# Performance work log

Measured on AMD Instinct MI355X. Metric: run time of the kernel, lower is better.

Reference implementation:

```python
import jax, jax.numpy as jnp
import numpy as np
from jax import lax

FIRE_RATE = 0.5       # forward() default fire_rate
INPUT_CHANNELS = 1    # module input_channels
EPS = 1e-5            # BatchNorm eps


def p4_conv_z2(x, w, b):
    """Z2 -> P4 group conv. x: [B,I,H,W], w: [O,I,k,k] -> [B,O,4,H,W]."""
    # rotate the spatial kernel by r*90deg for each of the 4 output orientations
    ws = jnp.stack([jnp.rot90(w, r, axes=(2, 3)) for r in range(4)], axis=1)  # [O,4,I,k,k]
    O, _, I, k, _ = ws.shape
    y = lax.conv_general_dilated(x, ws.reshape(O * 4, I, k, k), (1, 1), 'SAME',
                                 dimension_numbers=('NCHW', 'OIHW', 'NCHW'))
    B, _, H, W = x.shape
    return y.reshape(B, O, 4, H, W) + b[None, :, None, None, None]


def p4_conv_p4(x, w, b):
    """P4 -> P4 group conv. x: [B,I,4,H,W], w: [O,I,4,k,k] -> [B,O,4,H,W]."""
    # for output orientation r: cyclic-shift input-orientation axis by r and rotate spatially by r
    ws = jnp.stack([jnp.rot90(jnp.roll(w, r, axis=2), r, axes=(3, 4)) for r in range(4)],
                   axis=1)  # [O,4,I,4,k,k]
    O, _, I, _, k, _ = ws.shape
    B, _, _, H, W = x.shape
    y = lax.conv_general_dilated(x.reshape(B, I * 4, H, W),
                                 ws.reshape(O * 4, I * 4, k, k), (1, 1), 'SAME',
                                 dimension_numbers=('NCHW', 'OIHW', 'NCHW'))
    return y.reshape(B, O, 4, H, W) + b[None, :, None, None, None]


def _update(x_nhwc, w1, b1, gamma, beta, w2, b2, key):
    x = jnp.transpose(x_nhwc, (0, 3, 1, 2))            # [B,C,H,W]
    y = p4_conv_z2(x, w1, b1)                          # [B,Ch,4,H,W]
    # BatchNorm3d (batch stats, affine): normalize each channel over (B, rot, H, W)
    mu = jnp.mean(y, axis=(0, 2, 3, 4), keepdims=True)
    var = jnp.var(y, axis=(0, 2, 3, 4), keepdims=True)
    y = gamma[None, :, None, None, None] * (y - mu) * lax.rsqrt(var + EPS) \
        + beta[None, :, None, None, None]
    y = jax.nn.relu(y)
    dy = p4_conv_p4(y, w2, b2).mean(axis=2)            # mean over rotation axis -> [B,C,H,W]
    B, _, H, W = dy.shape
    mask = (jax.random.uniform(key, (B, 1, H, W), dtype=dy.dtype) > FIRE_RATE).astype(dy.dtype)
    x = x + dy * mask
    return jnp.transpose(x, (0, 2, 3, 1))              # back to [B,H,W,C]


def nca_forward(x, w1, b1, gamma, beta, w2, b2, steps):
    base_key = jax.random.key(42)
    for step in range(steps):
        x2 = _update(x, w1, b1, gamma, beta, w2, b2, jax.random.fold_in(base_key, step))
        # first input_channels are clamped to the original input
        x = jnp.concatenate((x[..., :INPUT_CHANNELS], x2[..., INPUT_CHANNELS:]), axis=-1)
    return x


def setup_inputs() -> dict:
    key = jax.random.key(0)
    ks = jax.random.split(key, 6)
    B, H, W = 8, 192, 192
    C = 16            # channel_n
    CH = 128 // 8     # base_hidden_size = hidden_size // 8
    K = 7             # kernel_size
    # fan-in scaled init (matches nn.Conv2d-style scaling)
    x = jax.random.normal(ks[0], (B, H, W, C), dtype=jnp.float32)
    w1 = jax.random.normal(ks[1], (CH, C, K, K), dtype=jnp.float32) / np.sqrt(C * K * K)
    b1 = jnp.zeros((CH,), dtype=jnp.float32)
    gamma = jnp.ones((CH,), dtype=jnp.float32)
    beta = jnp.zeros((CH,), dtype=jnp.float32)
    w2 = jax.random.normal(ks[2], (C, CH, 4, 1, 1), dtype=jnp.float32) / np.sqrt(CH * 4)
    b2 = jnp.zeros((C,), dtype=jnp.float32)
    return {"x": x, "w1": w1, "b1": b1, "gamma": gamma, "beta": beta,
            "w2": w2, "b2": b2, "steps": 10}


def reference(x, w1, b1, gamma, beta, w2, b2, steps):
    return nca_forward(x, w1, b1, gamma, beta, w2, b2, steps)
```

## Files before the change

kernel.cpp:

```cpp
#include <hip/hip_runtime.h>
#include <stdint.h>

#define HH 192
#define WW 192
#define BB 8
#define NSTEP 10
#define HWSZ (HH*WW)
#define NPIX (BB*HWSZ)
#define TILE_W 24
#define TILE_H 16
#define XROWS 22
#define XCOLS 30
#define RSU   488
#define XBUFU (XROWS*RSU)
#define NKS   25
#define NBLK  (8*12*8)

typedef _Float16 f16x8 __attribute__((ext_vector_type(8)));
typedef float    f32x4 __attribute__((ext_vector_type(4)));

typedef __attribute__((address_space(1))) const uint32_t glb_u32;
typedef __attribute__((address_space(3))) uint32_t lds_u32;

union PackU { ushort u[8]; uint4 v; };

__host__ __device__ inline void tf2x32(uint32_t k0, uint32_t k1,
                                       uint32_t x0, uint32_t x1,
                                       uint32_t &o0, uint32_t &o1) {
  const uint32_t k2 = k0 ^ k1 ^ 0x1BD11BDAu;
  x0 += k0; x1 += k1;
#define TFR(r) { x0 += x1; x1 = (x1 << (r)) | (x1 >> (32 - (r))); x1 ^= x0; }
  TFR(13) TFR(15) TFR(26) TFR(6)
  x0 += k1; x1 += k2 + 1u;
  TFR(17) TFR(29) TFR(16) TFR(24)
  x0 += k2; x1 += k0 + 2u;
  TFR(13) TFR(15) TFR(26) TFR(6)
  x0 += k0; x1 += k1 + 3u;
  TFR(17) TFR(29) TFR(16) TFR(24)
  x0 += k1; x1 += k2 + 4u;
  TFR(13) TFR(15) TFR(26) TFR(6)
  x0 += k2; x1 += k0 + 5u;
#undef TFR
  o0 = x0; o1 = x1;
}

__device__ inline void split2048(float v, ushort &h, ushort &l) {
  _Float16 hi = (_Float16)v;
  float r = (v - (float)hi) * 2048.0f;
  _Float16 lo = (_Float16)r;
  h = __builtin_bit_cast(ushort, hi);
  l = __builtin_bit_cast(ushort, lo);
}

__global__ void k_prep_wfrag(const float* __restrict__ w1,
                             ushort* __restrict__ wfh, ushort* __restrict__ wfl) {
  int idx = blockIdx.x * 256 + threadIdx.x;
  if (idx >= NKS * 4 * 64) return;
  const int lane = idx & 63;
  const int sm = idx >> 6;
  const int s = sm >> 2, mt = sm & 3;
  const int m = lane & 15, g = lane >> 4;
  const int j = mt * 16 + m, co = j >> 2, r = j & 3;
  const int t = 2 * s + (g >> 1);
  PackU ph, pl;
#pragma unroll
  for (int e = 0; e < 8; ++e) {
    const int ci = 8 * (g & 1) + e;
    float wv = 0.f;
    if (t < 49) {
      const int ky = t / 7, kx = t - (t / 7) * 7;
      int a = ky, b = kx;
      for (int i = 0; i < r; ++i) { int na = b, nb = 6 - a; a = na; b = nb; }
      wv = w1[((co * 16 + ci) * 7 + a) * 7 + b];
    }
    split2048(wv, ph.u[e], pl.u[e]);
  }
  ((uint4*)wfh)[sm * 64 + lane] = ph.v;
  ((uint4*)wfl)[sm * 64 + lane] = pl.v;
}

__global__ void k_prep_w2(const float* __restrict__ w2, float* __restrict__ wsum) {
  int idx = threadIdx.x;
  float s = 0.f;
  for (int t = 0; t < 4; ++t) s += w2[idx * 4 + t];
  wsum[idx] = 0.25f * s;
}

__global__ __launch_bounds__(512, 2) void k_conv1(
    const float* __restrict__ xsrc,
    const ushort* __restrict__ wfh,
    const ushort* __restrict__ wfl,
    const float* __restrict__ b1,
    float* __restrict__ y,
    float* __restrict__ partials)
{
  __shared__ __align__(16) ushort xsm[2 * XBUFU];
  __shared__ __align__(16) ushort abh[2][2048];
  __shared__ __align__(16) ushort abl[2][2048];
  __shared__ float red2[8][32];
  const int tid = threadIdx.x;
  const int lane = tid & 63, wid = tid >> 6;
  const int x0 = blockIdx.x * TILE_W, y0 = blockIdx.y * TILE_H;
  const int b = blockIdx.z;

  {
    const ushort* gsrc = ((wid < 4) ? wfh : wfl) + (wid & 3) * 512 + lane * 8;
    ushort* ldst = ((wid < 4) ? abh[0] : abl[0]) + (wid & 3) * 512;
    __builtin_amdgcn_global_load_lds((glb_u32*)gsrc, (lds_u32*)ldst, 16, 0, 0);
  }

  for (int p = tid; p < XROWS * XCOLS * 2; p += 512) {
    const int half = p & 1, t2 = p >> 1;
    const int lr = t2 / XCOLS, lc = t2 - (t2 / XCOLS) * XCOLS;
    const int gy = y0 + lr - 3, gx = x0 + lc - 3;
    float4 v0, v1;
    if ((unsigned)gy < (unsigned)HH && (unsigned)gx < (unsigned)WW) {
      const float4* px = (const float4*)(xsrc + ((size_t)b * HWSZ + (size_t)gy * WW + gx) * 16 + half * 8);
      v0 = px[0]; v1 = px[1];
    } else {
      v0 = v1 = make_float4(0.f, 0.f, 0.f, 0.f);
    }
    const float xv[8] = {v0.x, v0.y, v0.z, v0.w, v1.x, v1.y, v1.z, v1.w};
    PackU h, l;
#pragma unroll
    for (int c = 0; c < 8; ++c) split2048(xv[c], h.u[c], l.u[c]);
    const int ub = lr * RSU + lc * 16 + half * 8;
    *(uint4*)&xsm[ub] = h.v;
    *(uint4*)&xsm[XBUFU + ub] = l.v;
  }
  __syncthreads();

  const int n = lane & 15;
  const int q = lane >> 4;
  const int h = q & 1;
  const int bU0 = n * RSU + (3 * wid + 0) * 16 + h * 8;
  const int bU1 = bU0 + 16;
  const int bU2 = bU0 + 32;

  float bias[4];
#pragma unroll
  for (int mt = 0; mt < 4; ++mt) bias[mt] = b1[mt * 4 + q];

  f32x4 accH[3][4], accC[3][4];
#pragma unroll
  for (int st = 0; st < 3; ++st)
#pragma unroll
    for (int mt = 0; mt < 4; ++mt) {
      const float bv = bias[mt];
      accH[st][mt] = (f32x4){bv, bv, bv, bv};
      accC[st][mt] = (f32x4){0.f, 0.f, 0.f, 0.f};
    }

  f16x8 Ah[4], Al[4];
  f16x8 Bh[2][3], Bl[2][3];

  {
    const int off = (lane < 32) ? 0 : 16;
    Bh[0][0] = *(const f16x8*)&xsm[bU0 + off];
    Bl[0][0] = *(const f16x8*)&xsm[XBUFU + bU0 + off];
    Bh[0][1] = *(const f16x8*)&xsm[bU1 + off];
    Bl[0][1] = *(const f16x8*)&xsm[XBUFU + bU1 + off];
    Bh[0][2] = *(const f16x8*)&xsm[bU2 + off];
    Bl[0][2] = *(const f16x8*)&xsm[XBUFU + bU2 + off];
  }

#pragma unroll
  for (int s = 0; s < NKS; ++s) {
    const int cb = s & 1, nb = cb ^ 1;
    if (s < NKS - 1) {
      const ushort* gsrc = ((wid < 4) ? wfh : wfl) + (s + 1) * 2048 + (wid & 3) * 512 + lane * 8;
      ushort* ldst = ((wid < 4) ? abh[nb] : abl[nb]) + (wid & 3) * 512;
      __builtin_amdgcn_global_load_lds((glb_u32*)gsrc, (lds_u32*)ldst, 16, 0, 0);
    }
#pragma unroll
    for (int mt = 0; mt < 4; ++mt) Ah[mt] = *(const f16x8*)&abh[cb][mt * 512 + lane * 8];
#pragma unroll
    for (int mt = 0; mt < 4; ++mt) Al[mt] = *(const f16x8*)&abl[cb][mt * 512 + lane * 8];
    if (s < NKS - 1) {
      const int t0 = 2 * (s + 1), t1 = t0 + 1;
      const int o0 = (t0 / 7) * RSU + (t0 % 7) * 16;
      const int o1 = (t1 < 49) ? (t1 / 7) * RSU + (t1 % 7) * 16 : 0;
      const int off = (lane < 32) ? o0 : o1;
      Bh[nb][0] = *(const f16x8*)&xsm[bU0 + off];
      Bl[nb][0] = *(const f16x8*)&xsm[XBUFU + bU0 + off];
      Bh[nb][1] = *(const f16x8*)&xsm[bU1 + off];
      Bl[nb][1] = *(const f16x8*)&xsm[XBUFU + bU1 + off];
      Bh[nb][2] = *(const f16x8*)&xsm[bU2 + off];
      Bl[nb][2] = *(const f16x8*)&xsm[XBUFU + bU2 + off];
    }
    __builtin_amdgcn_sched_barrier(0);
    __builtin_amdgcn_s_setprio(1);
#pragma unroll
    for (int mt = 0; mt < 4; ++mt) {
#pragma unroll
      for (int st = 0; st < 3; ++st)
        accH[st][mt] = __builtin_amdgcn_mfma_f32_16x16x32_f16(Ah[mt], Bh[cb][st], accH[st][mt], 0, 0, 0);
    }
#pragma unroll
    for (int mt = 0; mt < 4; ++mt) {
#pragma unroll
      for (int st = 0; st < 3; ++st) {
        accC[st][mt] = __builtin_amdgcn_mfma_f32_16x16x32_f16(Ah[mt], Bl[cb][st], accC[st][mt], 0, 0, 0);
        accC[st][mt] = __builtin_amdgcn_mfma_f32_16x16x32_f16(Al[mt], Bh[cb][st], accC[st][mt], 0, 0, 0);
      }
    }
    __builtin_amdgcn_s_setprio(0);
    __builtin_amdgcn_sched_barrier(0);
    __syncthreads();
  }

  float sC[4] = {0.f, 0.f, 0.f, 0.f}, qC[4] = {0.f, 0.f, 0.f, 0.f};
#pragma unroll
  for (int st = 0; st < 3; ++st) {
    const size_t pix = (size_t)b * HWSZ + (size_t)(y0 + n) * WW + (x0 + 3 * wid + st);
#pragma unroll
    for (int mt = 0; mt < 4; ++mt) {
      f32x4 res = accH[st][mt] + accC[st][mt] * 4.8828125e-4f;
      *(float4*)(y + pix * 64 + mt * 16 + q * 4) =
          make_float4(res[0], res[1], res[2], res[3]);
#pragma unroll
      for (int r = 0; r < 4; ++r) { sC[mt] += res[r]; qC[mt] += res[r] * res[r]; }
    }
  }
#pragma unroll
  for (int mt = 0; mt < 4; ++mt) {
    float s = sC[mt], s2 = qC[mt];
#pragma unroll
    for (int off = 1; off <= 8; off <<= 1) {
      s += __shfl_xor(s, off); s2 += __shfl_xor(s2, off);
    }
    if (n == 0) {
      red2[wid][(mt * 4 + q) * 2] = s;
      red2[wid][(mt * 4 + q) * 2 + 1] = s2;
    }
  }
  __syncthreads();
  if (tid < 32) {
    float v = 0.f;
#pragma unroll
    for (int w2i = 0; w2i < 8; ++w2i) v += red2[w2i][tid];
    const int blk = (b * gridDim.y + blockIdx.y) * gridDim.x + blockIdx.x;
    partials[(size_t)blk * 32 + tid] = v;
  }
}

__global__ __launch_bounds__(256) void k_update(
    const float* __restrict__ xsrc,
    const float* __restrict__ y,
    const float* __restrict__ partials,
    const float* __restrict__ gamma, const float* __restrict__ beta,
    const float* __restrict__ wsum,
    const float* __restrict__ b2,
    float* __restrict__ xdst,
    uint32_t fk0, uint32_t fk1)
{
  __shared__ float redp[8][32];
  __shared__ float sss[32];
  __shared__ float sws[256];
  __shared__ float sb2[16];
  const int tid = threadIdx.x;
  sws[tid] = wsum[tid];
  if (tid < 16) sb2[tid] = b2[tid];

  {
    const int j = tid & 31, g = tid >> 5;
    float s = 0.f;
    for (int i = g; i < NBLK; i += 8) s += partials[(size_t)i * 32 + j];
    redp[g][j] = s;
  }
  __syncthreads();
  if (tid < 16) {
    float s1 = 0.f, s2 = 0.f;
#pragma unroll
    for (int g = 0; g < 8; ++g) { s1 += redp[g][2 * tid]; s2 += redp[g][2 * tid + 1]; }
    const float N = (float)BB * 4.f * HH * WW;
    const float mu = s1 / N;
    const float var = s2 / N - mu * mu;
    const float sc = gamma[tid] * rsqrtf(var + 1e-5f);
    sss[2 * tid]     = sc;
    sss[2 * tid + 1] = beta[tid] - mu * sc;
  }
  __syncthreads();

  const size_t pix = (size_t)blockIdx.x * 256 + tid;
  const float4* yp = (const float4*)(y + pix * 64);
  float ysum[16];
#pragma unroll
  for (int c = 0; c < 16; ++c) {
    const float4 v = yp[c];
    const float sc = sss[2 * c], sh = sss[2 * c + 1];
    ysum[c] = fmaxf(fmaf(sc, v.x, sh), 0.f) + fmaxf(fmaf(sc, v.y, sh), 0.f)
            + fmaxf(fmaf(sc, v.z, sh), 0.f) + fmaxf(fmaf(sc, v.w, sh), 0.f);
  }

  uint32_t h0, h1;
  tf2x32(fk0, fk1, 0u, (uint32_t)pix, h0, h1);
  const uint32_t bits = h0 ^ h1;
  const float u = __uint_as_float((bits >> 9) | 0x3f800000u) - 1.0f;
  const float m = (u > 0.5f) ? 1.0f : 0.0f;

  const float4* xp = (const float4*)(xsrc + pix * 16);
  float4* op = (float4*)(xdst + pix * 16);
#pragma unroll
  for (int qq = 0; qq < 4; ++qq) {
    const float4 xv = xp[qq];
    float d[4];
#pragma unroll
    for (int jj = 0; jj < 4; ++jj) {
      const int o = 4 * qq + jj;
      float s = sb2[o];
#pragma unroll
      for (int c = 0; c < 16; ++c) s = fmaf(sws[o * 16 + c], ysum[c], s);
      d[jj] = s;
    }
    float4 r;
    r.x = xv.x + d[0] * m;
    r.y = xv.y + d[1] * m;
    r.z = xv.z + d[2] * m;
    r.w = xv.w + d[3] * m;
    if (qq == 0) r.x = xv.x;
    op[qq] = r;
  }
}

extern "C" void kernel_launch(void* const* d_in, const int* in_sizes, int n_in,
                              void* d_out, int out_size, void* d_ws, size_t ws_size,
                              hipStream_t stream) {
  const float* x_in  = (const float*)d_in[0];
  const float* w1    = (const float*)d_in[1];
  const float* b1    = (const float*)d_in[2];
  const float* gamma = (const float*)d_in[3];
  const float* beta  = (const float*)d_in[4];
  const float* w2    = (const float*)d_in[5];
  const float* b2    = (const float*)d_in[6];
  float* out = (float*)d_out;

  float* ws       = (float*)d_ws;
  float* y        = ws;
  ushort* wfh     = (ushort*)(y + (size_t)NPIX * 64);
  ushort* wfl     = wfh + NKS * 2048;
  float* wsum     = (float*)(wfl + NKS * 2048);
  float* partials = wsum + 256;

  k_prep_wfrag<<<NKS, 256, 0, stream>>>(w1, wfh, wfl);
  k_prep_w2<<<1, 256, 0, stream>>>(w2, wsum);

  for (int s = 0; s < NSTEP; ++s) {
    const float* xsrc = (s == 0) ? x_in : out;
    k_conv1<<<dim3(WW / TILE_W, HH / TILE_H, BB), 512, 0, stream>>>(xsrc, wfh, wfl, b1, y, partials);
    uint32_t fk0, fk1;
    tf2x32(0u, 42u, 0u, (uint32_t)s, fk0, fk1);
    k_update<<<NPIX / 256, 256, 0, stream>>>(xsrc, y, partials, gamma, beta, wsum, b2, out, fk0, fk1);
  }
}
```

Baseline: 1.293 ms.

## Load conv weights directly into registers and hoist BN stat reduction into separate kernel

The conv kernel no longer stages weight fragments through LDS with global_load_lds and a per-step __syncthreads. Each wave instead loads its A fragments straight from global memory into double-buffered registers, which removes 25 block barriers per tile at the cost of more VGPRs and duplicated global/L2 reads across waves. The batch-norm statistic reduction, previously repeated by every k_update block over all partials, moves into a small k_bnstats kernel that writes scale and shift once per step. This adds one extra launch per step.

```diff
diff --git a/kernel.cpp b/kernel.cpp
--- a/kernel.cpp
+++ b/kernel.cpp
@@ -18,9 +18,6 @@
 
 typedef _Float16 f16x8 __attribute__((ext_vector_type(8)));
 typedef float    f32x4 __attribute__((ext_vector_type(4)));
-
-typedef __attribute__((address_space(1))) const uint32_t glb_u32;
-typedef __attribute__((address_space(3))) uint32_t lds_u32;
 
 union PackU { ushort u[8]; uint4 v; };
 
@@ -95,19 +92,11 @@
     float* __restrict__ partials)
 {
   __shared__ __align__(16) ushort xsm[2 * XBUFU];
-  __shared__ __align__(16) ushort abh[2][2048];
-  __shared__ __align__(16) ushort abl[2][2048];
   __shared__ float red2[8][32];
   const int tid = threadIdx.x;
   const int lane = tid & 63, wid = tid >> 6;
   const int x0 = blockIdx.x * TILE_W, y0 = blockIdx.y * TILE_H;
   const int b = blockIdx.z;
-
-  {
-    const ushort* gsrc = ((wid < 4) ? wfh : wfl) + (wid & 3) * 512 + lane * 8;
-    ushort* ldst = ((wid < 4) ? abh[0] : abl[0]) + (wid & 3) * 512;
-    __builtin_amdgcn_global_load_lds((glb_u32*)gsrc, (lds_u32*)ldst, 16, 0, 0);
-  }
 
   for (int p = tid; p < XROWS * XCOLS * 2; p += 512) {
     const int half = p & 1, t2 = p >> 1;
@@ -137,6 +126,9 @@
   const int bU1 = bU0 + 16;
   const int bU2 = bU0 + 32;
 
+  const f16x8* __restrict__ WAh = (const f16x8*)wfh;
+  const f16x8* __restrict__ WAl = (const f16x8*)wfl;
+
   float bias[4];
 #pragma unroll
   for (int mt = 0; mt < 4; ++mt) bias[mt] = b1[mt * 4 + q];
@@ -151,9 +143,14 @@
       accC[st][mt] = (f32x4){0.f, 0.f, 0.f, 0.f};
     }
 
-  f16x8 Ah[4], Al[4];
+  f16x8 Ah[2][4], Al[2][4];
   f16x8 Bh[2][3], Bl[2][3];
 
+#pragma unroll
+  for (int mt = 0; mt < 4; ++mt) {
+    Ah[0][mt] = WAh[mt * 64 + lane];
+    Al[0][mt] = WAl[mt * 64 + lane];
+  }
   {
     const int off = (lane < 32) ? 0 : 16;
     Bh[0][0] = *(const f16x8*)&xsm[bU0 + off];
@@ -168,15 +165,12 @@
   for (int s = 0; s < NKS; ++s) {
     const int cb = s & 1, nb = cb ^ 1;
     if (s < NKS - 1) {
-      const ushort* gsrc = ((wid < 4) ? wfh : wfl) + (s + 1) * 2048 + (wid & 3) * 512 + lane * 8;
-      ushort* ldst = ((wid < 4) ? abh[nb] : abl[nb]) + (wid & 3) * 512;
-      __builtin_amdgcn_global_load_lds((glb_u32*)gsrc, (lds_u32*)ldst, 16, 0, 0);
-    }
-#pragma unroll
-    for (int mt = 0; mt < 4; ++mt) Ah[mt] = *(const f16x8*)&abh[cb][mt * 512 + lane * 8];
-#pragma unroll
-    for (int mt = 0; mt < 4; ++mt) Al[mt] = *(const f16x8*)&abl[cb][mt * 512 + lane * 8];
-    if (s < NKS - 1) {
+#pragma unroll
+      for (int mt = 0; mt < 4; ++mt) {
+        const int f = ((s + 1) * 4 + mt) * 64 + lane;
+        Ah[nb][mt] = WAh[f];
+        Al[nb][mt] = WAl[f];
+      }
       const int t0 = 2 * (s + 1), t1 = t0 + 1;
       const int o0 = (t0 / 7) * RSU + (t0 % 7) * 16;
       const int o1 = (t1 < 49) ? (t1 / 7) * RSU + (t1 % 7) * 16 : 0;
@@ -194,19 +188,18 @@
     for (int mt = 0; mt < 4; ++mt) {
 #pragma unroll
       for (int st = 0; st < 3; ++st)
-        accH[st][mt] = __builtin_amdgcn_mfma_f32_16x16x32_f16(Ah[mt], Bh[cb][st], accH[st][mt], 0, 0, 0);
+        accH[st][mt] = __builtin_amdgcn_mfma_f32_16x16x32_f16(Ah[cb][mt], Bh[cb][st], accH[st][mt], 0, 0, 0);
     }
 #pragma unroll
     for (int mt = 0; mt < 4; ++mt) {
 #pragma unroll
       for (int st = 0; st < 3; ++st) {
-        accC[st][mt] = __builtin_amdgcn_mfma_f32_16x16x32_f16(Ah[mt], Bl[cb][st], accC[st][mt], 0, 0, 0);
-        accC[st][mt] = __builtin_amdgcn_mfma_f32_16x16x32_f16(Al[mt], Bh[cb][st], accC[st][mt], 0, 0, 0);
+        accC[st][mt] = __builtin_amdgcn_mfma_f32_16x16x32_f16(Ah[cb][mt], Bl[cb][st], accC[st][mt], 0, 0, 0);
+        accC[st][mt] = __builtin_amdgcn_mfma_f32_16x16x32_f16(Al[cb][mt], Bh[cb][st], accC[st][mt], 0, 0, 0);
       }
     }
     __builtin_amdgcn_s_setprio(0);
     __builtin_amdgcn_sched_barrier(0);
-    __syncthreads();
   }
 
   float sC[4] = {0.f, 0.f, 0.f, 0.f}, qC[4] = {0.f, 0.f, 0.f, 0.f};
@@ -244,42 +237,52 @@
   }
 }
 
+__global__ __launch_bounds__(256) void k_bnstats(
+    const float* __restrict__ partials,
+    const float* __restrict__ gamma, const float* __restrict__ beta,
+    float* __restrict__ stats)
+{
+  const int c = blockIdx.x;
+  const int tid = threadIdx.x;
+  float s = 0.f, s2 = 0.f;
+  for (int i = tid; i < NBLK; i += 256) {
+    s  += partials[(size_t)i * 32 + 2 * c];
+    s2 += partials[(size_t)i * 32 + 2 * c + 1];
+  }
+  __shared__ float rs[256], rs2[256];
+  rs[tid] = s; rs2[tid] = s2;
+  __syncthreads();
+  for (int off = 128; off > 0; off >>= 1) {
+    if (tid < off) { rs[tid] += rs[tid + off]; rs2[tid] += rs2[tid + off]; }
+    __syncthreads();
+  }
+  if (tid == 0) {
+    const float N = (float)BB * 4.f * HH * WW;
+    const float mu = rs[0] / N;
+    const float var = rs2[0] / N - mu * mu;
+    const float rstd = rsqrtf(var + 1e-5f);
+    const float sc = gamma[c] * rstd;
+    stats[2 * c]     = sc;
+    stats[2 * c + 1] = beta[c] - mu * sc;
+  }
+}
+
 __global__ __launch_bounds__(256) void k_update(
     const float* __restrict__ xsrc,
     const float* __restrict__ y,
-    const float* __restrict__ partials,
-    const float* __restrict__ gamma, const float* __restrict__ beta,
+    const float* __restrict__ stats,
     const float* __restrict__ wsum,
     const float* __restrict__ b2,
     float* __restrict__ xdst,
     uint32_t fk0, uint32_t fk1)
 {
-  __shared__ float redp[8][32];
   __shared__ float sss[32];
   __shared__ float sws[256];
   __shared__ float sb2[16];
   const int tid = threadIdx.x;
   sws[tid] = wsum[tid];
+  if (tid < 32) sss[tid] = stats[tid];
   if (tid < 16) sb2[tid] = b2[tid];
-
-  {
-    const int j = tid & 31, g = tid >> 5;
-    float s = 0.f;
-    for (int i = g; i < NBLK; i += 8) s += partials[(size_t)i * 32 + j];
-    redp[g][j] = s;
-  }
-  __syncthreads();
-  if (tid < 16) {
-    float s1 = 0.f, s2 = 0.f;
-#pragma unroll
-    for (int g = 0; g < 8; ++g) { s1 += redp[g][2 * tid]; s2 += redp[g][2 * tid + 1]; }
-    const float N = (float)BB * 4.f * HH * WW;
-    const float mu = s1 / N;
-    const float var = s2 / N - mu * mu;
-    const float sc = gamma[tid] * rsqrtf(var + 1e-5f);
-    sss[2 * tid]     = sc;
-    sss[2 * tid + 1] = beta[tid] - mu * sc;
-  }
   __syncthreads();
 
   const size_t pix = (size_t)blockIdx.x * 256 + tid;
@@ -341,6 +344,7 @@
   ushort* wfl     = wfh + NKS * 2048;
   float* wsum     = (float*)(wfl + NKS * 2048);
   float* partials = wsum + 256;
+  float* stats    = partials + NBLK * 32;
 
   k_prep_wfrag<<<NKS, 256, 0, stream>>>(w1, wfh, wfl);
   k_prep_w2<<<1, 256, 0, stream>>>(w2, wsum);
@@ -348,8 +352,9 @@
   for (int s = 0; s < NSTEP; ++s) {
     const float* xsrc = (s == 0) ? x_in : out;
     k_conv1<<<dim3(WW / TILE_W, HH / TILE_H, BB), 512, 0, stream>>>(xsrc, wfh, wfl, b1, y, partials);
+    k_bnstats<<<16, 256, 0, stream>>>(partials, gamma, beta, stats);
     uint32_t fk0, fk1;
     tf2x32(0u, 42u, 0u, (uint32_t)s, fk0, fk1);
-    k_update<<<NPIX / 256, 256, 0, stream>>>(xsrc, y, partials, gamma, beta, wsum, b2, out, fk0, fk1);
-  }
-}
+    k_update<<<NPIX / 256, 256, 0, stream>>>(xsrc, y, stats, wsum, b2, out, fk0, fk1);
+  }
+}
```

Result: faster. 1.101 ms (-14.9%).
